# Performance work log

Hardware: AMD Instinct MI355X
Metric: run time of the kernel (lower is better)

Reference implementation:

```python
import jax, jax.numpy as jnp
import numpy as np

N_EMBD = 768
N_HEAD = 12

def setup_inputs() -> dict:
    key = jax.random.key(0)
    k_x, k_wa, k_ba, k_wp, k_bp = jax.random.split(key, 5)
    C = N_EMBD
    scale = 1.0 / np.sqrt(C)
    return {
        "x": jax.random.normal(k_x, (2, 4096, C), dtype=jnp.float32),
        "W_attn": jax.random.normal(k_wa, (C, 3 * C), dtype=jnp.float32) * scale,
        "b_attn": jax.random.normal(k_ba, (3 * C,), dtype=jnp.float32) * 0.01,
        "W_proj": jax.random.normal(k_wp, (C, C), dtype=jnp.float32) * scale,
        "b_proj": jax.random.normal(k_bp, (C,), dtype=jnp.float32) * 0.01,
    }

def reference(x, W_attn, b_attn, W_proj, b_proj) -> jnp.ndarray:
    B, T, C = x.shape
    H = N_HEAD
    D = C // H  # head dim
    qkv = x @ W_attn + b_attn                     # [B,T,3C]
    q, k, v = jnp.split(qkv, 3, axis=-1)
    # [B,T,C] -> [B,H,T,D]
    q = q.reshape(B, T, H, D).transpose(0, 2, 1, 3)
    k = k.reshape(B, T, H, D).transpose(0, 2, 1, 3)
    v = v.reshape(B, T, H, D).transpose(0, 2, 1, 3)
    scores = jnp.einsum("bhqd,bhkd->bhqk", q, k) * (1.0 / jnp.sqrt(jnp.float32(D)))
    attn = jax.nn.softmax(scores, axis=-1)        # dropout p=0.0 -> identity
    y = jnp.einsum("bhqk,bhkd->bhqd", attn, v)    # [B,H,T,D]
    y = y.transpose(0, 2, 1, 3).reshape(B, T, C)
    return y @ W_proj + b_proj
```

## Files before the change

kernel.cpp:

```cpp
#include <hip/hip_runtime.h>
#include <stdint.h>

#define NB 2
#define NT 4096
#define NC 768
#define NH 12
#define ND 64
#define NBT (NB*NT)
#define NQKV (3*NC)

typedef _Float16 half_t;
typedef __attribute__((ext_vector_type(8))) _Float16 f16x8;
typedef __attribute__((ext_vector_type(4))) _Float16 f16x4;
typedef __attribute__((ext_vector_type(2))) __fp16 fp16x2;
typedef __attribute__((ext_vector_type(4))) float f32x4;

#define MFMA16(a,b,c) __builtin_amdgcn_mfma_f32_16x16x32_f16((a),(b),(c),0,0,0)

__device__ __forceinline__ void load_lds16(const void* g, void* l) {
    auto gp = reinterpret_cast<__attribute__((address_space(1))) char*>(reinterpret_cast<uintptr_t>(g));
    auto lp = reinterpret_cast<__attribute__((address_space(3))) char*>(reinterpret_cast<uintptr_t>(l));
    __builtin_amdgcn_global_load_lds(gp, lp, 16, 0, 0);
}

#define PACK_BLKS ((NBT * NC / 4) / 256)
#define WA_TILES ((NC / 32) * (NQKV / 32))
#define WP_TILES ((NC / 32) * (NC / 32))
#define PREP_BLKS (PACK_BLKS + WA_TILES + WP_TILES)

__global__ __launch_bounds__(256) void k_prep(const float* __restrict__ x, half_t* __restrict__ xh,
                                              const float* __restrict__ Wa, half_t* __restrict__ Wat,
                                              const float* __restrict__ Wp, half_t* __restrict__ Wpt) {
    const int bid = blockIdx.x, tid = threadIdx.x;
    if (bid < PACK_BLKS) {
        const int i = bid * 256 + tid;
        float4 f = reinterpret_cast<const float4*>(x)[i];
        f16x4 h;
        h[0] = (half_t)f.x; h[1] = (half_t)f.y; h[2] = (half_t)f.z; h[3] = (half_t)f.w;
        reinterpret_cast<f16x4*>(xh)[i] = h;
        return;
    }
    __shared__ half_t tile[32][36];
    const float* in; half_t* out; int N, kt, nt;
    if (bid < PACK_BLKS + WA_TILES) {
        const int t = bid - PACK_BLKS;
        in = Wa; out = Wat; N = NQKV;
        kt = t / (NQKV / 32); nt = t - kt * (NQKV / 32);
    } else {
        const int t = bid - PACK_BLKS - WA_TILES;
        in = Wp; out = Wpt; N = NC;
        kt = t / (NC / 32); nt = t - kt * (NC / 32);
    }
    const int k0 = kt * 32, n0 = nt * 32;
    {
        const int r = tid >> 3, c = (tid & 7) * 4;
        float4 f = *reinterpret_cast<const float4*>(&in[(size_t)(k0 + r) * N + n0 + c]);
        tile[r][c] = (half_t)f.x; tile[r][c + 1] = (half_t)f.y;
        tile[r][c + 2] = (half_t)f.z; tile[r][c + 3] = (half_t)f.w;
    }
    __syncthreads();
    {
        const int rn = tid >> 3, ck = (tid & 7) * 4;
        f16x4 u;
        u[0] = tile[ck][rn]; u[1] = tile[ck + 1][rn];
        u[2] = tile[ck + 2][rn]; u[3] = tile[ck + 3][rn];
        *reinterpret_cast<f16x4*>(&out[(size_t)(n0 + rn) * NC + k0 + ck]) = u;
    }
}

template<int OUTF32>
__global__ __launch_bounds__(256) void k_gemm(const half_t* __restrict__ A, const half_t* __restrict__ Bt,
                                              const float* __restrict__ bias, void* __restrict__ out, int N,
                                              half_t* __restrict__ Vt) {
    __shared__ half_t As[2][128 * 32];
    __shared__ half_t Bs[2][128 * 32];
    const int tid = threadIdx.x;
    const int lane = tid & 63, w = tid >> 6;
    const int m0 = blockIdx.x * 128, n0 = blockIdx.y * 128;
    const int wm = (w >> 1) * 64, wn = (w & 1) * 64;
    const int lr = lane & 15, lk = (lane >> 4) * 8;

    f32x4 acc[4][4];
#pragma unroll
    for (int a = 0; a < 4; ++a)
#pragma unroll
        for (int bq = 0; bq < 4; ++bq) acc[a][bq] = (f32x4){0.f, 0.f, 0.f, 0.f};

    const int c0 = tid, c1 = 256 + tid;
    const int ldsbase = (tid & ~63) * 16;
    const half_t* A0 = A  + (size_t)(m0 + (c0 >> 2)) * NC + (c0 & 3) * 8;
    const half_t* A1 = A  + (size_t)(m0 + (c1 >> 2)) * NC + (c1 & 3) * 8;
    const half_t* B0 = Bt + (size_t)(n0 + (c0 >> 2)) * NC + (c0 & 3) * 8;
    const half_t* B1 = Bt + (size_t)(n0 + (c1 >> 2)) * NC + (c1 & 3) * 8;

    auto stage = [&](int buf, int k0) {
        load_lds16(A0 + k0, (char*)&As[buf][0] + ldsbase);
        load_lds16(B0 + k0, (char*)&Bs[buf][0] + ldsbase);
        load_lds16(A1 + k0, (char*)&As[buf][0] + 4096 + ldsbase);
        load_lds16(B1 + k0, (char*)&Bs[buf][0] + 4096 + ldsbase);
    };

    stage(0, 0);
    __syncthreads();
    int cur = 0;

    for (int ks = 0; ks < 24; ++ks) {
        if (ks < 23) stage(cur ^ 1, (ks + 1) * 32);
        f16x8 af[4], bf[4];
#pragma unroll
        for (int mi = 0; mi < 4; ++mi)
            af[mi] = *reinterpret_cast<const f16x8*>(&As[cur][(wm + mi * 16 + lr) * 32 + lk]);
#pragma unroll
        for (int ni = 0; ni < 4; ++ni)
            bf[ni] = *reinterpret_cast<const f16x8*>(&Bs[cur][(wn + ni * 16 + lr) * 32 + lk]);
#pragma unroll
        for (int mi = 0; mi < 4; ++mi)
#pragma unroll
            for (int ni = 0; ni < 4; ++ni)
                acc[mi][ni] = MFMA16(af[mi], bf[ni], acc[mi][ni]);
        __syncthreads();
        cur ^= 1;
    }

    const int rg = (lane >> 4) * 4;

    if (Vt != nullptr && n0 >= 2 * NC) {
        half_t* q = (w < 2) ? &As[w][0] : &Bs[w - 2][0];
#pragma unroll
        for (int ni = 0; ni < 4; ++ni) {
            const int d = ni * 16 + lr;
            const float bv = bias[n0 + wn + d];
            const int xsw = (d & 7) << 3;
#pragma unroll
            for (int mi = 0; mi < 4; ++mi) {
                const int t0 = mi * 16 + rg;
                union { f16x4 v; fp16x2 hh[2]; } o;
                o.hh[0] = __builtin_amdgcn_cvt_pkrtz(acc[mi][ni][0] + bv, acc[mi][ni][1] + bv);
                o.hh[1] = __builtin_amdgcn_cvt_pkrtz(acc[mi][ni][2] + bv, acc[mi][ni][3] + bv);
                *reinterpret_cast<f16x4*>(&q[d * 64 + (t0 ^ xsw)]) = o.v;
            }
        }
        __syncthreads();
        const int M0 = m0 + wm;
        const int bh = (M0 >> 12) * NH + ((n0 - 2 * NC + wn) >> 6);
        half_t* vbase = Vt + (size_t)bh * ND * NT + (M0 & (NT - 1));
#pragma unroll
        for (int k2 = 0; k2 < 8; ++k2) {
            const int d = 8 * k2 + (lane >> 3);
            const int tt = (lane & 7) * 8;
            f16x8 val = *reinterpret_cast<const f16x8*>(&q[d * 64 + (tt ^ ((d & 7) << 3))]);
            *reinterpret_cast<f16x8*>(&vbase[(size_t)d * NT + tt]) = val;
        }
        return;
    }

#pragma unroll
    for (int ni = 0; ni < 4; ++ni) {
        const int gn = n0 + wn + ni * 16 + lr;
        const float bv = bias[gn];
#pragma unroll
        for (int mi = 0; mi < 4; ++mi)
#pragma unroll
            for (int i = 0; i < 4; ++i) {
                const size_t gm = (size_t)(m0 + wm + mi * 16 + rg + i);
                const float v = acc[mi][ni][i] + bv;
                if (OUTF32) reinterpret_cast<float*>(out)[gm * N + gn] = v;
                else        reinterpret_cast<half_t*>(out)[gm * N + gn] = (half_t)v;
            }
    }
}

struct __align__(16) AttnSmem {
    union {
        struct { half_t K[2][64 * 64]; half_t V[2][64 * 64]; } m;
        struct { float y[2][64][64]; float l[2][64][4]; } r;
    };
};

__global__ __launch_bounds__(256, 3) void k_attn(const half_t* __restrict__ qkv, const half_t* __restrict__ Vt,
                                                 half_t* __restrict__ Y) {
    __shared__ AttnSmem sm;
    const int tid = threadIdx.x, lane = tid & 63, w = tid >> 6;
    const int qw = w & 1, kw = w >> 1;
    const int lr = lane & 15, g = lane >> 4;
    const int qt = blockIdx.x, bh = blockIdx.y;
    const int b = bh / NH, h = bh - b * NH;
    const half_t* Qp = qkv + (size_t)b * NT * NQKV + h * ND;
    const half_t* Kp = Qp + NC;
    const half_t* Vbase = Vt + (size_t)bh * ND * NT;
    const int q0 = qt * 128 + qw * 64;

    const int sr = tid >> 3;
    const int colh = (((tid & 7) << 3)) ^ ((sr & 7) << 3);
    const int wub = (tid & ~63) * 16;

    f16x8 aq[4][2];
    const half_t cch = (half_t)(0.125f * 1.4426950408889634f);
#pragma unroll
    for (int qf = 0; qf < 4; ++qf)
#pragma unroll
        for (int dh = 0; dh < 2; ++dh) {
            aq[qf][dh] = *reinterpret_cast<const f16x8*>(&Qp[(size_t)(q0 + qf * 16 + lr) * NQKV + dh * 32 + g * 8]);
#pragma unroll
            for (int j = 0; j < 8; ++j) aq[qf][dh][j] = aq[qf][dh][j] * cch;
        }

    const int swk = (lr & 7) << 3;
    const int cA = (g * 8) ^ swk;
    const int cB = (32 + g * 8) ^ swk;
    const int psw = lr & 7;
    const int goff = (g & 1) << 2;
    const int vcol[2] = { (((g >> 1) + 4 * kw + 0) ^ psw) * 8 + goff,
                          (((g >> 1) + 4 * kw + 2) ^ psw) * 8 + goff };

    f32x4 y[4][4];
#pragma unroll
    for (int qf = 0; qf < 4; ++qf)
#pragma unroll
        for (int df = 0; df < 4; ++df) y[qf][df] = (f32x4){0.f, 0.f, 0.f, 0.f};
    float l_[4] = {0.f, 0.f, 0.f, 0.f};

    auto stagebuf = [&](int buf, const half_t* Ks, const half_t* Vs) {
        char* kdst = (char*)&sm.m.K[buf][0] + wub;
        char* vdst = (char*)&sm.m.V[buf][0] + wub;
        load_lds16(Ks, kdst);
        load_lds16(Ks + (size_t)32 * NQKV, kdst + 4096);
        load_lds16(Vs, vdst);
        load_lds16(Vs + (size_t)32 * NT, vdst + 4096);
    };

    const half_t* ksrc = Kp + (size_t)sr * NQKV + colh;
    const half_t* vsrc = Vbase + (size_t)sr * NT + colh;
    stagebuf(0, ksrc, vsrc);
    ksrc += (size_t)64 * NQKV;
    vsrc += 64;
    __syncthreads();
    int cur = 0;
    const int stb = 2 * kw;

    for (int t = 0; t < NT / 64; ++t) {
        if (t < NT / 64 - 1) {
            stagebuf(cur ^ 1, ksrc, vsrc);
            ksrc += (size_t)64 * NQKV;
            vsrc += 64;
        }

        f32x4 s[4][2];
#pragma unroll
        for (int qf = 0; qf < 4; ++qf) { s[qf][0] = (f32x4){0.f,0.f,0.f,0.f}; s[qf][1] = (f32x4){0.f,0.f,0.f,0.f}; }
        const half_t* Kc = &sm.m.K[cur][0];
        __builtin_amdgcn_s_setprio(1);
#pragma unroll
        for (int sl = 0; sl < 2; ++sl) {
            const int row = (stb + sl) * 16 + lr;
            f16x8 bk0 = *reinterpret_cast<const f16x8*>(&Kc[row * 64 + cA]);
            s[0][sl] = MFMA16(bk0, aq[0][0], s[0][sl]);
            s[1][sl] = MFMA16(bk0, aq[1][0], s[1][sl]);
            s[2][sl] = MFMA16(bk0, aq[2][0], s[2][sl]);
            s[3][sl] = MFMA16(bk0, aq[3][0], s[3][sl]);
            f16x8 bk1 = *reinterpret_cast<const f16x8*>(&Kc[row * 64 + cB]);
            s[0][sl] = MFMA16(bk1, aq[0][1], s[0][sl]);
            s[1][sl] = MFMA16(bk1, aq[1][1], s[1][sl]);
            s[2][sl] = MFMA16(bk1, aq[2][1], s[2][sl]);
            s[3][sl] = MFMA16(bk1, aq[3][1], s[3][sl]);
        }
        __builtin_amdgcn_s_setprio(0);

        f16x8 pb[4];
#pragma unroll
        for (int qf = 0; qf < 4; ++qf) {
            float ps = 0.f;
            union { f16x8 v; fp16x2 h[4]; } u;
#pragma unroll
            for (int hs = 0; hs < 2; ++hs) {
                const float p0 = __builtin_amdgcn_exp2f(s[qf][hs][0]);
                const float p1 = __builtin_amdgcn_exp2f(s[qf][hs][1]);
                const float p2 = __builtin_amdgcn_exp2f(s[qf][hs][2]);
                const float p3 = __builtin_amdgcn_exp2f(s[qf][hs][3]);
                u.h[2 * hs]     = __builtin_amdgcn_cvt_pkrtz(p0, p1);
                u.h[2 * hs + 1] = __builtin_amdgcn_cvt_pkrtz(p2, p3);
                ps += (p0 + p1) + (p2 + p3);
            }
            pb[qf] = u.v;
            l_[qf] += ps;
        }

        const half_t* Vc = &sm.m.V[cur][0];
        __builtin_amdgcn_s_setprio(1);
#pragma unroll
        for (int df = 0; df < 4; ++df) {
            const half_t* vrow = &Vc[(df * 16 + lr) * 64];
            union { f16x8 v; f16x4 q[2]; } va;
            va.q[0] = *reinterpret_cast<const f16x4*>(vrow + vcol[0]);
            va.q[1] = *reinterpret_cast<const f16x4*>(vrow + vcol[1]);
            y[0][df] = MFMA16(va.v, pb[0], y[0][df]);
            y[1][df] = MFMA16(va.v, pb[1], y[1][df]);
            y[2][df] = MFMA16(va.v, pb[2], y[2][df]);
            y[3][df] = MFMA16(va.v, pb[3], y[3][df]);
        }
        __builtin_amdgcn_s_setprio(0);

        __syncthreads();
        cur ^= 1;
    }

    if (kw == 1) {
#pragma unroll
        for (int qf = 0; qf < 4; ++qf)
#pragma unroll
            for (int df = 0; df < 4; ++df) {
                const int jb = (qf * 16 + df * 4) ^ ((lane & 7) << 2);
                *reinterpret_cast<f32x4*>(&sm.r.y[qw][lane][jb]) = y[qf][df];
            }
#pragma unroll
        for (int qf = 0; qf < 4; ++qf) sm.r.l[qw][lane][qf] = l_[qf];
    }
    __syncthreads();
    if (kw == 0) {
#pragma unroll
        for (int qf = 0; qf < 4; ++qf) {
#pragma unroll
            for (int df = 0; df < 4; ++df) {
                const int jb = (qf * 16 + df * 4) ^ ((lane & 7) << 2);
                const f32x4 yp = *reinterpret_cast<const f32x4*>(&sm.r.y[qw][lane][jb]);
                y[qf][df] += yp;
            }
            float l = l_[qf] + sm.r.l[qw][lane][qf];
            l += __shfl_xor(l, 16);
            l += __shfl_xor(l, 32);
            const float rl = 1.f / l;
            half_t* Yp = Y + (size_t)(b * NT + q0 + qf * 16 + lr) * NC + h * ND + g * 4;
#pragma unroll
            for (int df = 0; df < 4; ++df) {
                union { f16x4 v; fp16x2 hh[2]; } o;
                o.hh[0] = __builtin_amdgcn_cvt_pkrtz(y[qf][df][0] * rl, y[qf][df][1] * rl);
                o.hh[1] = __builtin_amdgcn_cvt_pkrtz(y[qf][df][2] * rl, y[qf][df][3] * rl);
                *reinterpret_cast<f16x4*>(Yp + df * 16) = o.v;
            }
        }
    }
}

extern "C" void kernel_launch(void* const* d_in, const int* in_sizes, int n_in,
                              void* d_out, int out_size, void* d_ws, size_t ws_size,
                              hipStream_t stream) {
    const float* x  = (const float*)d_in[0];
    const float* Wa = (const float*)d_in[1];
    const float* ba = (const float*)d_in[2];
    const float* Wp = (const float*)d_in[3];
    const float* bp = (const float*)d_in[4];
    float* out = (float*)d_out;

    char* ws = (char*)d_ws;
    half_t* xh   = (half_t*)ws; ws += (size_t)NBT * NC * 2;
    half_t* Wat  = (half_t*)ws; ws += (size_t)NQKV * NC * 2;
    half_t* Wpt  = (half_t*)ws; ws += (size_t)NC * NC * 2;
    half_t* qkvh = (half_t*)ws; ws += (size_t)NBT * NQKV * 2;
    half_t* vt   = (half_t*)ws; ws += (size_t)NB * NH * ND * NT * 2;
    half_t* yh   = (half_t*)ws; ws += (size_t)NBT * NC * 2;

    k_prep<<<PREP_BLKS, 256, 0, stream>>>(x, xh, Wa, Wat, Wp, Wpt);
    k_gemm<0><<<dim3(NBT / 128, NQKV / 128), 256, 0, stream>>>(xh, Wat, ba, qkvh, NQKV, vt);
    k_attn<<<dim3(NT / 128, NB * NH), 256, 0, stream>>>(qkvh, vt, yh);
    k_gemm<1><<<dim3(NBT / 128, NC / 128), 256, 0, stream>>>(yh, Wpt, bp, out, NC, nullptr);
}
```

Measured before the change: 194.3 us.

## Use wider 128x192 tiles in a dedicated QKV GEMM kernel

Splits the QKV projection into its own kernel, `k_gemm0`. Each block now computes a 128x192 output tile with 4x6 MFMA fragments per wave, which increases reuse of the staged A tile and cuts the grid from 1152 to 768 blocks. The V-transpose epilogue is reworked to handle 96 columns per wave in two passes through per-wave LDS scratch, and `__launch_bounds__(256,3)` is added. The cost is more accumulator registers per thread and more LDS per block, which may limit occupancy. The output-projection GEMM is simplified to an fp32-only, non-templated kernel.

```diff
diff --git a/kernel.cpp b/kernel.cpp
--- a/kernel.cpp
+++ b/kernel.cpp
@@ -68,10 +68,110 @@
     }
 }
 
-template<int OUTF32>
+__global__ __launch_bounds__(256, 3) void k_gemm0(const half_t* __restrict__ A, const half_t* __restrict__ Bt,
+                                                  const float* __restrict__ bias, half_t* __restrict__ out,
+                                                  half_t* __restrict__ Vt) {
+    __shared__ half_t As[2][128 * 32];
+    __shared__ half_t Bs[2][192 * 32];
+    const int tid = threadIdx.x;
+    const int lane = tid & 63, w = tid >> 6;
+    const int m0 = blockIdx.x * 128, n0 = blockIdx.y * 192;
+    const int wm = (w >> 1) * 64, wn = (w & 1) * 96;
+    const int lr = lane & 15, lk = (lane >> 4) * 8;
+
+    f32x4 acc[4][6];
+#pragma unroll
+    for (int a = 0; a < 4; ++a)
+#pragma unroll
+        for (int bq = 0; bq < 6; ++bq) acc[a][bq] = (f32x4){0.f, 0.f, 0.f, 0.f};
+
+    const int ldsbase = (tid & ~63) * 16;
+    const half_t* Arow = A  + (size_t)(m0 + (tid >> 2)) * NC + (tid & 3) * 8;
+    const half_t* Brow = Bt + (size_t)(n0 + (tid >> 2)) * NC + (tid & 3) * 8;
+
+    auto stage = [&](int buf, int k0) {
+        load_lds16(Arow + k0,                    (char*)&As[buf][0] + ldsbase);
+        load_lds16(Arow + (size_t)64 * NC + k0,  (char*)&As[buf][0] + 4096 + ldsbase);
+        load_lds16(Brow + k0,                    (char*)&Bs[buf][0] + ldsbase);
+        load_lds16(Brow + (size_t)64 * NC + k0,  (char*)&Bs[buf][0] + 4096 + ldsbase);
+        load_lds16(Brow + (size_t)128 * NC + k0, (char*)&Bs[buf][0] + 8192 + ldsbase);
+    };
+
+    stage(0, 0);
+    __syncthreads();
+    int cur = 0;
+
+    for (int ks = 0; ks < 24; ++ks) {
+        if (ks < 23) stage(cur ^ 1, (ks + 1) * 32);
+        f16x8 af[4];
+#pragma unroll
+        for (int mi = 0; mi < 4; ++mi)
+            af[mi] = *reinterpret_cast<const f16x8*>(&As[cur][(wm + mi * 16 + lr) * 32 + lk]);
+#pragma unroll
+        for (int ni = 0; ni < 6; ++ni) {
+            f16x8 bf = *reinterpret_cast<const f16x8*>(&Bs[cur][(wn + ni * 16 + lr) * 32 + lk]);
+#pragma unroll
+            for (int mi = 0; mi < 4; ++mi)
+                acc[mi][ni] = MFMA16(af[mi], bf, acc[mi][ni]);
+        }
+        __syncthreads();
+        cur ^= 1;
+    }
+
+    const int rg = (lane >> 4) * 4;
+
+    if (n0 >= 2 * NC) {
+        half_t* q = (w < 2) ? (half_t*)((char*)&As[0][0] + w * 8192)
+                            : (half_t*)((char*)&Bs[0][0] + (w - 2) * 8192);
+        const int M0 = m0 + wm;
+        const int bb = M0 >> 12;
+        const int trow = M0 & (NT - 1);
+#pragma unroll
+        for (int p = 0; p < 2; ++p) {
+#pragma unroll
+            for (int n3 = 0; n3 < 3; ++n3) {
+                const int ni = p * 3 + n3;
+                const int c = n3 * 16 + lr;
+                const float bv = bias[n0 + wn + p * 48 + c];
+                const int xsw = (c & 7) << 3;
+#pragma unroll
+                for (int mi = 0; mi < 4; ++mi) {
+                    const int t0 = mi * 16 + rg;
+                    union { f16x4 v; fp16x2 hh[2]; } o;
+                    o.hh[0] = __builtin_amdgcn_cvt_pkrtz(acc[mi][ni][0] + bv, acc[mi][ni][1] + bv);
+                    o.hh[1] = __builtin_amdgcn_cvt_pkrtz(acc[mi][ni][2] + bv, acc[mi][ni][3] + bv);
+                    *reinterpret_cast<f16x4*>(&q[c * 64 + (t0 ^ xsw)]) = o.v;
+                }
+            }
+#pragma unroll
+            for (int j = 0; j < 6; ++j) {
+                const int cl = j * 8 + (lane >> 3);
+                const int tt = (lane & 7) * 8;
+                f16x8 val = *reinterpret_cast<const f16x8*>(&q[cl * 64 + (tt ^ ((cl & 7) << 3))]);
+                const int dcol = n0 - 2 * NC + wn + p * 48 + cl;
+                const int bh = bb * NH + (dcol >> 6);
+                *reinterpret_cast<f16x8*>(&Vt[((size_t)bh * ND + (dcol & 63)) * NT + trow + tt]) = val;
+            }
+        }
+        return;
+    }
+
+#pragma unroll
+    for (int ni = 0; ni < 6; ++ni) {
+        const int gn = n0 + wn + ni * 16 + lr;
+        const float bv = bias[gn];
+#pragma unroll
+        for (int mi = 0; mi < 4; ++mi)
+#pragma unroll
+            for (int i = 0; i < 4; ++i) {
+                const size_t gm = (size_t)(m0 + wm + mi * 16 + rg + i);
+                out[gm * NQKV + gn] = (half_t)(acc[mi][ni][i] + bv);
+            }
+    }
+}
+
 __global__ __launch_bounds__(256) void k_gemm(const half_t* __restrict__ A, const half_t* __restrict__ Bt,
-                                              const float* __restrict__ bias, void* __restrict__ out, int N,
-                                              half_t* __restrict__ Vt) {
+                                              const float* __restrict__ bias, float* __restrict__ out, int N) {
     __shared__ half_t As[2][128 * 32];
     __shared__ half_t Bs[2][128 * 32];
     const int tid = threadIdx.x;
@@ -123,37 +223,6 @@
     }
 
     const int rg = (lane >> 4) * 4;
-
-    if (Vt != nullptr && n0 >= 2 * NC) {
-        half_t* q = (w < 2) ? &As[w][0] : &Bs[w - 2][0];
-#pragma unroll
-        for (int ni = 0; ni < 4; ++ni) {
-            const int d = ni * 16 + lr;
-            const float bv = bias[n0 + wn + d];
-            const int xsw = (d & 7) << 3;
-#pragma unroll
-            for (int mi = 0; mi < 4; ++mi) {
-                const int t0 = mi * 16 + rg;
-                union { f16x4 v; fp16x2 hh[2]; } o;
-                o.hh[0] = __builtin_amdgcn_cvt_pkrtz(acc[mi][ni][0] + bv, acc[mi][ni][1] + bv);
-                o.hh[1] = __builtin_amdgcn_cvt_pkrtz(acc[mi][ni][2] + bv, acc[mi][ni][3] + bv);
-                *reinterpret_cast<f16x4*>(&q[d * 64 + (t0 ^ xsw)]) = o.v;
-            }
-        }
-        __syncthreads();
-        const int M0 = m0 + wm;
-        const int bh = (M0 >> 12) * NH + ((n0 - 2 * NC + wn) >> 6);
-        half_t* vbase = Vt + (size_t)bh * ND * NT + (M0 & (NT - 1));
-#pragma unroll
-        for (int k2 = 0; k2 < 8; ++k2) {
-            const int d = 8 * k2 + (lane >> 3);
-            const int tt = (lane & 7) * 8;
-            f16x8 val = *reinterpret_cast<const f16x8*>(&q[d * 64 + (tt ^ ((d & 7) << 3))]);
-            *reinterpret_cast<f16x8*>(&vbase[(size_t)d * NT + tt]) = val;
-        }
-        return;
-    }
-
 #pragma unroll
     for (int ni = 0; ni < 4; ++ni) {
         const int gn = n0 + wn + ni * 16 + lr;
@@ -163,9 +232,7 @@
 #pragma unroll
             for (int i = 0; i < 4; ++i) {
                 const size_t gm = (size_t)(m0 + wm + mi * 16 + rg + i);
-                const float v = acc[mi][ni][i] + bv;
-                if (OUTF32) reinterpret_cast<float*>(out)[gm * N + gn] = v;
-                else        reinterpret_cast<half_t*>(out)[gm * N + gn] = (half_t)v;
+                out[gm * N + gn] = acc[mi][ni][i] + bv;
             }
     }
 }
@@ -360,7 +427,7 @@
     half_t* yh   = (half_t*)ws; ws += (size_t)NBT * NC * 2;
 
     k_prep<<<PREP_BLKS, 256, 0, stream>>>(x, xh, Wa, Wat, Wp, Wpt);
-    k_gemm<0><<<dim3(NBT / 128, NQKV / 128), 256, 0, stream>>>(xh, Wat, ba, qkvh, NQKV, vt);
+    k_gemm0<<<dim3(NBT / 128, NQKV / 192), 256, 0, stream>>>(xh, Wat, ba, qkvh, vt);
     k_attn<<<dim3(NT / 128, NB * NH), 256, 0, stream>>>(qkvh, vt, yh);
-    k_gemm<1><<<dim3(NBT / 128, NC / 128), 256, 0, stream>>>(yh, Wpt, bp, out, NC, nullptr);
-}
+    k_gemm<<<dim3(NBT / 128, NC / 128), 256, 0, stream>>>(yh, Wpt, bp, out, NC);
+}
```

Result: faster. 184.5 us (-5.1%).
